# Performance work log

Hardware: AMD Instinct MI355X
Metric: run time of the kernel (lower is better)

The kernel has to match this reference:

```python
import jax, jax.numpy as jnp
import numpy as np

EPS = 1.1  # GIN epsilon from GINLayer(1.1, dim)
N_GIN = 4

def setup_inputs() -> dict:
    key = jax.random.key(0)
    ks = jax.random.split(key, 24)
    R, F_IN, H1, D = 1048576, 64, 256, 128
    N, E, B, A1, T = 100000, 1600000, 4096, 256, 16
    s = 0.05
    inp = {}
    inp['bulk'] = jax.random.normal(ks[0], (R, F_IN), dtype=jnp.float32)
    inp['seg_ids'] = jnp.sort(jax.random.randint(ks[1], (R,), 0, N))
    inp['edge_src'] = jax.random.randint(ks[2], (E,), 0, N)
    inp['edge_dst'] = jax.random.randint(ks[3], (E,), 0, N)
    inp['root_idx'] = jax.random.randint(ks[4], (B,), 0, N)
    inp['num_nodes'] = N
    # feature extractor: Linear(64,256)+ReLU, Linear(256,128)+ReLU
    inp['W1'] = jax.random.normal(ks[5], (F_IN, H1), dtype=jnp.float32) * s
    inp['b1'] = jnp.zeros((H1,), jnp.float32)
    inp['W2'] = jax.random.normal(ks[6], (H1, D), dtype=jnp.float32) * s
    inp['b2'] = jnp.zeros((D,), jnp.float32)
    # 4 GIN layers, dim D -> D
    inp['gin_W'] = jax.random.normal(ks[7], (N_GIN, D, D), dtype=jnp.float32) * s
    inp['gin_b'] = jnp.zeros((N_GIN, D), jnp.float32)
    # actor: Linear(128,256)+ReLU, Linear(256,16)+ReLU, Softmax
    inp['Wa1'] = jax.random.normal(ks[8], (D, A1), dtype=jnp.float32) * s
    inp['ba1'] = jnp.zeros((A1,), jnp.float32)
    inp['Wa2'] = jax.random.normal(ks[9], (A1, T), dtype=jnp.float32) * s
    inp['ba2'] = jnp.zeros((T,), jnp.float32)
    # critic: Linear(128,256)+ReLU, Linear(256,1)
    inp['Wc1'] = jax.random.normal(ks[10], (D, A1), dtype=jnp.float32) * s
    inp['bc1'] = jnp.zeros((A1,), jnp.float32)
    inp['Wc2'] = jax.random.normal(ks[11], (A1, 1), dtype=jnp.float32) * s
    inp['bc2'] = jnp.zeros((1,), jnp.float32)
    return inp

def reference(bulk, seg_ids, edge_src, edge_dst, root_idx, num_nodes,
              W1, b1, W2, b2, gin_W, gin_b, Wa1, ba1, Wa2, ba2, Wc1, bc1, Wc2, bc2):
    # feature extractor over all rows
    h = jax.nn.relu(bulk @ W1 + b1)
    h = jax.nn.relu(h @ W2 + b2)  # [R, D]
    # per-dataset mean aggregation (self.aggregator over split groups)
    sums = jax.ops.segment_sum(h, seg_ids, num_segments=num_nodes)
    counts = jax.ops.segment_sum(jnp.ones((h.shape[0],), h.dtype), seg_ids, num_segments=num_nodes)
    node_h = sums / jnp.maximum(counts, 1.0)[:, None]  # [N, D]
    # GIN message passing: h_v <- relu(W ((1+eps) h_v + sum_{child u} h_u) + b)
    for i in range(N_GIN):
        agg = jax.ops.segment_sum(node_h[edge_src], edge_dst, num_segments=num_nodes)
        node_h = jax.nn.relu(((1.0 + EPS) * node_h + agg) @ gin_W[i] + gin_b[i])
    X = node_h[root_idx]  # [B, D] current-node representations
    act = jax.nn.softmax(jax.nn.relu(jax.nn.relu(X @ Wa1 + ba1) @ Wa2 + ba2), axis=-1)
    crit = (jax.nn.relu(X @ Wc1 + bc1) @ Wc2 + bc2).squeeze(-1)
    return (act, crit)
```

## Files before the change

### kernel.cpp

```cpp
#include <hip/hip_runtime.h>
#include <math.h>

#define R_ROWS 1048576
#define F_IN   64
#define H1     256
#define D      128
#define NN     100000
#define NE     1600000
#define NB     4096
#define A1     256
#define NTOK   16
#define N_GIN  4
#define FE_ROWS 64

typedef short short8 __attribute__((ext_vector_type(8)));
typedef float f32x4  __attribute__((ext_vector_type(4)));
typedef unsigned int uintx4 __attribute__((ext_vector_type(4)));

__device__ __forceinline__ ushort f2bf(float x) {
    uint u = __builtin_bit_cast(uint, x);
    u += 0x7FFFu + ((u >> 16) & 1u);
    return (ushort)(u >> 16);
}
__device__ __forceinline__ float bf2f(ushort h) {
    uint u = ((uint)h) << 16;
    return __builtin_bit_cast(float, u);
}
__device__ __forceinline__ uint cvtpk(float lo, float hi) {
    uint r;
    asm("v_cvt_pk_bf16_f32 %0, %1, %2" : "=v"(r) : "v"(lo), "v"(hi));
    return r;
}
__device__ __forceinline__ float lo16f(uint p) { return __builtin_bit_cast(float, p << 16); }
__device__ __forceinline__ float hi16f(uint p) { return __builtin_bit_cast(float, p & 0xFFFF0000u); }

__device__ __forceinline__ f32x4 mm(short8 a, short8 b, f32x4 c) {
    return __builtin_amdgcn_mfma_f32_16x16x32_bf16(a, b, c, 0, 0, 0);
}
__device__ __forceinline__ void acc_add(f32x4& L, f32x4& H, const uintx4 p) {
    L[0] += lo16f(p[0]); H[0] += hi16f(p[0]);
    L[1] += lo16f(p[1]); H[1] += hi16f(p[1]);
    L[2] += lo16f(p[2]); H[2] += hi16f(p[2]);
    L[3] += lo16f(p[3]); H[3] += hi16f(p[3]);
}

__device__ __forceinline__ void pack_one(const float* __restrict__ W, int Ndim,
                                         int f, int lane, ushort* __restrict__ out)
{
    const int NTn = Ndim >> 4;
    const int kt = f / NTn, nt = f - kt * NTn;
    const int k0 = kt * 32 + (lane >> 4) * 8;
    const int n = nt * 16 + (lane & 15);
    uintx4 Hv, Lv;
    #pragma unroll
    for (int jj = 0; jj < 4; ++jj) {
        const float x0 = W[(k0 + 2 * jj) * Ndim + n];
        const float x1 = W[(k0 + 2 * jj + 1) * Ndim + n];
        const ushort h0 = f2bf(x0), l0 = f2bf(x0 - bf2f(h0));
        const ushort h1u = f2bf(x1), l1 = f2bf(x1 - bf2f(h1u));
        Hv[jj] = (uint)h0 | ((uint)h1u << 16);
        Lv[jj] = (uint)l0 | ((uint)l1 << 16);
    }
    *reinterpret_cast<uintx4*>(&out[((f * 2 + 0) * 64 + lane) * 8]) = Hv;
    *reinterpret_cast<uintx4*>(&out[((f * 2 + 1) * 64 + lane) * 8]) = Lv;
}

__global__ __launch_bounds__(256) void pack_all(
    const float* __restrict__ W1, const float* __restrict__ W2,
    const float* __restrict__ ginW, const float* __restrict__ Wa1,
    const float* __restrict__ Wc1, const float* __restrict__ Wa2,
    ushort* __restrict__ W1p, ushort* __restrict__ W2p, ushort* __restrict__ Gp,
    ushort* __restrict__ Wa1p, ushort* __restrict__ Wc1p, ushort* __restrict__ Wa2p,
    int* __restrict__ deg, int* __restrict__ mark, int* __restrict__ cnt)
{
    const int bid = blockIdx.x;
    if (bid < 90) {
        const int fid = bid * 4 + (threadIdx.x >> 6);
        const int lane = threadIdx.x & 63;
        if (fid < 32) pack_one(W1, H1, fid, lane, W1p);
        else if (fid < 96) pack_one(W2, D, fid - 32, lane, W2p);
        else if (fid < 224) {
            const int l = (fid - 96) >> 5;
            pack_one(ginW + (long)l * D * D, D, (fid - 96) & 31, lane, Gp + (long)l * 32768);
        } else if (fid < 288) pack_one(Wa1, A1, fid - 224, lane, Wa1p);
        else if (fid < 352) pack_one(Wc1, A1, fid - 288, lane, Wc1p);
        else if (fid < 360) pack_one(Wa2, NTOK, fid - 352, lane, Wa2p);
    } else {
        const int zb = bid - 90;
        const int idx0 = (zb * 256 + threadIdx.x) * 4;
        #pragma unroll
        for (int k = 0; k < 4; ++k) {
            const int idx = idx0 + k;
            if (idx < NN) deg[idx] = 0;
            else if (idx < 2 * NN) mark[idx - NN] = 0;
        }
        if (bid == 90 && threadIdx.x == 0) cnt[0] = 0;
    }
}

__global__ __launch_bounds__(256, 4) void fe_mfma(
    const float* __restrict__ bulk, const int* __restrict__ seg,
    const ushort* __restrict__ W1p, const float* __restrict__ b1,
    const ushort* __restrict__ W2p, const float* __restrict__ b2,
    float* __restrict__ sums)
{
    __shared__ __align__(16) uint smem_u[10240];
    char* Ab  = (char*)smem_u;
    char* h1b = Ab + 8192;
    float* h2 = (float*)smem_u;

    const int t = threadIdx.x;
    const int lane = t & 63;
    const int w = t >> 6;
    const long r0 = (long)blockIdx.x * FE_ROWS;

    #pragma unroll
    for (int i = 0; i < 4; ++i) {
        const int gid = t + i * 256;
        const int row = gid >> 4;
        const int c4 = (gid & 15) * 4;
        const float4 v = *reinterpret_cast<const float4*>(&bulk[(r0 + row) * F_IN + c4]);
        uint2 pk; pk.x = cvtpk(v.x, v.y); pk.y = cvtpk(v.z, v.w);
        const int byteoff = row * 128 + ((c4 * 2) ^ ((row & 7) << 4));
        *reinterpret_cast<uint2*>(Ab + byteoff) = pk;
    }
    __syncthreads();

    const f32x4 zz = {0.f, 0.f, 0.f, 0.f};
    f32x4 acc1[4][4];
    #pragma unroll
    for (int mtl = 0; mtl < 4; ++mtl)
        #pragma unroll
        for (int ntb = 0; ntb < 4; ++ntb) acc1[mtl][ntb] = zz;

    #pragma unroll
    for (int kt = 0; kt < 2; ++kt) {
        short8 aw[4];
        #pragma unroll
        for (int mtl = 0; mtl < 4; ++mtl) {
            const int f = kt * 16 + (w * 4 + mtl);
            aw[mtl] = *reinterpret_cast<const short8*>(&W1p[((f * 2 + 0) * 64 + lane) * 8]);
        }
        short8 bh[4];
        #pragma unroll
        for (int ntb = 0; ntb < 4; ++ntb) {
            const int row = ntb * 16 + (lane & 15);
            const int k0 = kt * 32 + (lane >> 4) * 8;
            bh[ntb] = *reinterpret_cast<const short8*>(Ab + (row * 128 + ((k0 * 2) ^ ((row & 7) << 4))));
        }
        #pragma unroll
        for (int mtl = 0; mtl < 4; ++mtl)
            #pragma unroll
            for (int ntb = 0; ntb < 4; ++ntb)
                acc1[mtl][ntb] = mm(aw[mtl], bh[ntb], acc1[mtl][ntb]);
    }

    #pragma unroll
    for (int mtl = 0; mtl < 4; ++mtl) {
        const int hcb = w * 64 + mtl * 16 + (lane >> 4) * 4;
        const float4 bv = *reinterpret_cast<const float4*>(&b1[hcb]);
        #pragma unroll
        for (int ntb = 0; ntb < 4; ++ntb) {
            const int hr = (lane & 15) + ntb * 16;
            const float v0 = fmaxf(acc1[mtl][ntb][0] + bv.x, 0.f);
            const float v1 = fmaxf(acc1[mtl][ntb][1] + bv.y, 0.f);
            const float v2 = fmaxf(acc1[mtl][ntb][2] + bv.z, 0.f);
            const float v3 = fmaxf(acc1[mtl][ntb][3] + bv.w, 0.f);
            uint2 pk; pk.x = cvtpk(v0, v1); pk.y = cvtpk(v2, v3);
            const int byteoff = (hr * 512 + hcb * 2) ^ ((hr & 7) << 4);
            *reinterpret_cast<uint2*>(h1b + byteoff) = pk;
        }
    }
    __syncthreads();

    float b2v[2];
    #pragma unroll
    for (int ntl = 0; ntl < 2; ++ntl) b2v[ntl] = b2[w * 32 + ntl * 16 + (lane & 15)];
    f32x4 acc2[4][2];
    #pragma unroll
    for (int mt = 0; mt < 4; ++mt) { acc2[mt][0] = zz; acc2[mt][1] = zz; }

    #pragma unroll
    for (int kt = 0; kt < 8; ++kt) {
        short8 bw2[2][2];
        #pragma unroll
        for (int ntl = 0; ntl < 2; ++ntl)
            #pragma unroll
            for (int p = 0; p < 2; ++p) {
                const int f = kt * 8 + (w * 2 + ntl);
                bw2[ntl][p] = *reinterpret_cast<const short8*>(&W2p[((f * 2 + p) * 64 + lane) * 8]);
            }
        short8 ah[4];
        #pragma unroll
        for (int mt = 0; mt < 4; ++mt) {
            const int row = mt * 16 + (lane & 15);
            const int k0 = kt * 32 + (lane >> 4) * 8;
            ah[mt] = *reinterpret_cast<const short8*>(h1b + ((row * 512 + k0 * 2) ^ ((row & 7) << 4)));
        }
        #pragma unroll
        for (int mt = 0; mt < 4; ++mt)
            #pragma unroll
            for (int ntl = 0; ntl < 2; ++ntl) {
                acc2[mt][ntl] = mm(ah[mt], bw2[ntl][0], acc2[mt][ntl]);
                acc2[mt][ntl] = mm(ah[mt], bw2[ntl][1], acc2[mt][ntl]);
            }
    }
    __syncthreads();

    #pragma unroll
    for (int mt = 0; mt < 4; ++mt)
        #pragma unroll
        for (int ntl = 0; ntl < 2; ++ntl)
            #pragma unroll
            for (int r = 0; r < 4; ++r) {
                const int row = mt * 16 + (lane >> 4) * 4 + r;
                const int col = w * 32 + ntl * 16 + (lane & 15);
                h2[row * 132 + col] = fmaxf(acc2[mt][ntl][r] + b2v[ntl], 0.f);
            }
    __syncthreads();

    {
        const int g = t >> 7;
        const int c = t & 127;
        const int base = g * 32;
        const long rb = r0 + base;
        const int prev = (rb == 0) ? -1 : seg[rb - 1];
        const int nxt = (rb + 32 >= R_ROWS) ? -1 : seg[rb + 32];
        int cur = seg[rb];
        float run = 0.f;
        int runstart = 0;
        #pragma unroll 1
        for (int r = 0; r < 32; ++r) {
            const int s = seg[rb + r];
            if (s != cur) {
                if (runstart != 0 || cur != prev) sums[(long)cur * D + c] = run;
                else atomicAdd(&sums[(long)cur * D + c], run);
                cur = s; run = 0.f; runstart = r;
            }
            run += h2[(base + r) * 132 + c];
        }
        if ((runstart != 0 || cur != prev) && cur != nxt) sums[(long)cur * D + c] = run;
        else atomicAdd(&sums[(long)cur * D + c], run);
    }
}

__global__ __launch_bounds__(256) void start_kernel(const int* __restrict__ seg,
                                                    int* __restrict__ start)
{
    const int n = blockIdx.x * 256 + threadIdx.x;
    if (n > NN) return;
    int lo = 0, hi = R_ROWS;
    #pragma unroll 1
    while (lo < hi) {
        const int mid = (lo + hi) >> 1;
        if (seg[mid] < n) lo = mid + 1; else hi = mid;
    }
    start[n] = lo;
}

__global__ __launch_bounds__(256) void divide_bf(
    const float* __restrict__ sums, const int* __restrict__ start,
    uint* __restrict__ hbf)
{
    const long i = (long)blockIdx.x * 256 + threadIdx.x;
    if (i < (long)NN * 64) {
        const int n = (int)(i >> 6), u = (int)(i & 63);
        const int cA = (u & 15) + (u >> 4) * 32;
        const float inv = 1.f / fmaxf((float)(start[n + 1] - start[n]), 1.f);
        const float vA = sums[(long)n * D + cA] * inv;
        const float vB = sums[(long)n * D + cA + 16] * inv;
        hbf[i] = cvtpk(vA, vB);
    }
}

__global__ __launch_bounds__(256) void hist_kernel(const int* __restrict__ edst,
                                                   int* __restrict__ deg)
{
    const int e = blockIdx.x * 256 + threadIdx.x;
    if (e < NE) atomicAdd(&deg[edst[e]], 1);
}

#define SCHUNK 2048
__global__ __launch_bounds__(256) void scan_reduce(const int* __restrict__ deg,
                                                   int* __restrict__ partials, int n)
{
    __shared__ int sdata[256];
    const int b = blockIdx.x, t = threadIdx.x;
    const int base = b * SCHUNK;
    int sum = 0;
    for (int i = t; i < SCHUNK; i += 256) {
        const int idx = base + i;
        sum += (idx < n) ? deg[idx] : 0;
    }
    sdata[t] = sum; __syncthreads();
    for (int s = 128; s > 0; s >>= 1) {
        if (t < s) sdata[t] += sdata[t + s];
        __syncthreads();
    }
    if (t == 0) partials[b] = sdata[0];
}

__global__ __launch_bounds__(256) void scan_write(const int* __restrict__ deg,
                                                  const int* __restrict__ partials,
                                                  int nchunks,
                                                  int* __restrict__ offsets,
                                                  int* __restrict__ cursor, int n)
{
    __shared__ int sdata[256];
    __shared__ int base_sh;
    const int b = blockIdx.x, t = threadIdx.x;
    if (t < 64) {
        int v = (t < b && t < nchunks) ? partials[t] : 0;
        #pragma unroll
        for (int d2 = 1; d2 < 64; d2 <<= 1) v += __shfl_xor(v, d2);
        if (t == 0) base_sh = v;
    }
    const int base = b * SCHUNK;
    int loc[8]; int s = 0;
    #pragma unroll
    for (int j = 0; j < 8; ++j) {
        const int idx = base + t * 8 + j;
        const int v = (idx < n) ? deg[idx] : 0;
        loc[j] = s; s += v;
    }
    sdata[t] = s; __syncthreads();
    for (int d = 1; d < 256; d <<= 1) {
        const int v = (t >= d) ? sdata[t - d] : 0;
        __syncthreads();
        sdata[t] += v;
        __syncthreads();
    }
    const int excl = (t == 0) ? 0 : sdata[t - 1];
    const int tbase = base_sh + excl;
    #pragma unroll
    for (int j = 0; j < 8; ++j) {
        const int idx = base + t * 8 + j;
        if (idx < n) {
            const int o = tbase + loc[j];
            offsets[idx] = o;
            cursor[idx] = o;
        }
    }
}

__global__ __launch_bounds__(256) void scatter_edges(const int* __restrict__ esrc,
                                                     const int* __restrict__ edst,
                                                     int* __restrict__ cursor,
                                                     int* __restrict__ csr_src)
{
    const int e = blockIdx.x * 256 + threadIdx.x;
    if (e < NE) {
        const int d = edst[e];
        const int p = atomicAdd(&cursor[d], 1);
        csr_src[p] = esrc[e];
    }
}

__global__ __launch_bounds__(256) void mark_kernel(
    const int* __restrict__ root, const int* __restrict__ offsets,
    const int* __restrict__ deg, const int* __restrict__ csr,
    int* __restrict__ mark)
{
    const int b = blockIdx.x * 256 + threadIdx.x;
    if (b < NB) {
        const int n = root[b];
        mark[n] = 1;
        const int off = offsets[n], dg = deg[n];
        for (int j = 0; j < dg; ++j) mark[csr[off + j]] = 1;
    }
}

__global__ __launch_bounds__(256) void compact_kernel(
    const int* __restrict__ mark, int* __restrict__ list, int* __restrict__ cnt)
{
    const int n = blockIdx.x * 256 + threadIdx.x;
    if (n < NN && mark[n]) {
        const int p = atomicAdd(cnt, 1);
        list[p] = n;
    }
}

template<int MODE>
__global__ __launch_bounds__(256, 8) void gin_kernel(
    const uint* __restrict__ hbf, const int* __restrict__ offsets,
    const int* __restrict__ deg, const int* __restrict__ csr,
    const ushort* __restrict__ Wp, const float* __restrict__ bvec,
    uint* __restrict__ outbuf,
    const int* __restrict__ list, const int* __restrict__ cnt,
    const int* __restrict__ root)
{
    __shared__ __align__(16) char ylds[64 * 256];
    __shared__ int nid[64];
    const int t = threadIdx.x, lane = t & 63, w = t >> 6;
    const int h = lane >> 5;
    const int q2 = (lane >> 4) & 1;
    const int m = lane & 15;
    const int q = lane >> 4;
    const int r0 = blockIdx.x * 64;
    const int CNT = (MODE == 1) ? cnt[0] : 0;
    if (MODE == 1 && r0 >= CNT) return;

    #pragma unroll 1
    for (int i = 0; i < 8; ++i) {
        const int row = w * 16 + i * 2 + h;
        int n = -1;
        if (MODE == 0) {
            const int nn = r0 + row;
            if (nn < NN) n = nn;
        } else if (MODE == 1) {
            const int idx = r0 + row;
            if (idx < CNT) n = list[idx];
        } else {
            n = root[r0 + row];
        }
        if (MODE == 1 && (lane & 31) == 0) nid[row] = n;
        f32x4 accL = {0.f, 0.f, 0.f, 0.f};
        f32x4 accH = {0.f, 0.f, 0.f, 0.f};
        if (n >= 0) {
            const uintx4 sp = *reinterpret_cast<const uintx4*>(&hbf[(long)n * 64 + 4 * m]);
            const float sc = (q2 == 0) ? 2.1f : 0.f;
            accL[0] = sc * lo16f(sp[0]); accH[0] = sc * hi16f(sp[0]);
            accL[1] = sc * lo16f(sp[1]); accH[1] = sc * hi16f(sp[1]);
            accL[2] = sc * lo16f(sp[2]); accH[2] = sc * hi16f(sp[2]);
            accL[3] = sc * lo16f(sp[3]); accH[3] = sc * hi16f(sp[3]);
            const int off = offsets[n];
            const int dg = deg[n];
            const int dg2 = dg >> 1;
            int jj = 0;
            for (; jj + 4 <= dg2; jj += 4) {
                const int b0 = off + 2 * jj + q2;
                const int s0 = csr[b0], s1 = csr[b0 + 2], s2 = csr[b0 + 4], s3 = csr[b0 + 6];
                const uintx4 p0 = *reinterpret_cast<const uintx4*>(&hbf[(long)s0 * 64 + 4 * m]);
                const uintx4 p1 = *reinterpret_cast<const uintx4*>(&hbf[(long)s1 * 64 + 4 * m]);
                const uintx4 p2 = *reinterpret_cast<const uintx4*>(&hbf[(long)s2 * 64 + 4 * m]);
                const uintx4 p3 = *reinterpret_cast<const uintx4*>(&hbf[(long)s3 * 64 + 4 * m]);
                acc_add(accL, accH, p0);
                acc_add(accL, accH, p1);
                acc_add(accL, accH, p2);
                acc_add(accL, accH, p3);
            }
            for (; jj < dg2; ++jj) {
                const int s = csr[off + 2 * jj + q2];
                const uintx4 p = *reinterpret_cast<const uintx4*>(&hbf[(long)s * 64 + 4 * m]);
                acc_add(accL, accH, p);
            }
            if ((dg & 1) && q2 == 0) {
                const int s = csr[off + dg - 1];
                const uintx4 p = *reinterpret_cast<const uintx4*>(&hbf[(long)s * 64 + 4 * m]);
                acc_add(accL, accH, p);
            }
        }
        #pragma unroll
        for (int e = 0; e < 4; ++e) {
            accL[e] += __shfl_xor(accL[e], 16);
            accH[e] += __shfl_xor(accH[e], 16);
        }
        const int swz = (row & 7) << 4;
        #pragma unroll
        for (int e = 0; e < 2; ++e) {
            const int u = 4 * m + 2 * q2 + e;
            const int cA = (u & 15) + (u >> 4) * 32;
            const uint pk = cvtpk(accL[2 * q2 + e], accH[2 * q2 + e]);
            *reinterpret_cast<ushort*>(ylds + ((row * 256 + cA * 2) ^ swz)) = (ushort)pk;
            *reinterpret_cast<ushort*>(ylds + ((row * 256 + (cA + 16) * 2) ^ swz)) = (ushort)(pk >> 16);
        }
    }

    short8 bw0[2];
    #pragma unroll
    for (int ntl = 0; ntl < 2; ++ntl) {
        const int f = w * 2 + ntl;
        bw0[ntl] = *reinterpret_cast<const short8*>(&Wp[((f * 2 + 0) * 64 + lane) * 8]);
    }
    __syncthreads();

    const f32x4 zz = {0.f, 0.f, 0.f, 0.f};
    f32x4 acc[4][2];
    #pragma unroll
    for (int mt = 0; mt < 4; ++mt) { acc[mt][0] = zz; acc[mt][1] = zz; }

    #pragma unroll
    for (int kt = 0; kt < 4; ++kt) {
        short8 bw[2];
        if (kt == 0) { bw[0] = bw0[0]; bw[1] = bw0[1]; }
        else {
            #pragma unroll
            for (int ntl = 0; ntl < 2; ++ntl) {
                const int f = kt * 8 + (w * 2 + ntl);
                bw[ntl] = *reinterpret_cast<const short8*>(&Wp[((f * 2 + 0) * 64 + lane) * 8]);
            }
        }
        #pragma unroll
        for (int mt = 0; mt < 4; ++mt) {
            const int row = mt * 16 + m;
            const int k0 = kt * 32 + q * 8;
            const short8 ah = *reinterpret_cast<const short8*>(
                ylds + ((row * 256 + k0 * 2) ^ ((row & 7) << 4)));
            acc[mt][0] = mm(ah, bw[0], acc[mt][0]);
            acc[mt][1] = mm(ah, bw[1], acc[mt][1]);
        }
    }

    const float bv0 = bvec[w * 32 + m];
    const float bv1 = bvec[w * 32 + 16 + m];
    #pragma unroll
    for (int mt = 0; mt < 4; ++mt)
        #pragma unroll
        for (int r = 0; r < 4; ++r) {
            const int grow_row = mt * 16 + q * 4 + r;
            const float v0 = fmaxf(acc[mt][0][r] + bv0, 0.f);
            const float v1 = fmaxf(acc[mt][1][r] + bv1, 0.f);
            const uint pk = cvtpk(v0, v1);
            if (MODE == 0) {
                const long nout = r0 + grow_row;
                if (nout < NN) outbuf[nout * 64 + w * 16 + m] = pk;
            } else if (MODE == 1) {
                if (r0 + grow_row < CNT) {
                    const long nout = nid[grow_row];
                    outbuf[nout * 64 + w * 16 + m] = pk;
                }
            } else {
                outbuf[(long)(r0 + grow_row) * 64 + w * 16 + m] = pk;
            }
        }
}

__global__ __launch_bounds__(256) void head_mfma(
    const uint* __restrict__ Xbf,
    const ushort* __restrict__ Wa1p, const float* __restrict__ ba1,
    const ushort* __restrict__ Wa2p, const float* __restrict__ ba2,
    const ushort* __restrict__ Wc1p, const float* __restrict__ bc1,
    const float* __restrict__ Wc2, const float* __restrict__ bc2,
    float* __restrict__ out_act, float* __restrict__ out_crit)
{
    __shared__ __align__(16) char Xp[64 * 256];
    __shared__ __align__(16) char a1p[64 * 512];
    const int t = threadIdx.x, lane = t & 63, w = t >> 6;
    const int r0 = blockIdx.x * 64;
    const f32x4 zz = {0.f, 0.f, 0.f, 0.f};

    {
        const int row = t >> 2;
        const int ug = (t & 3) * 16;
        const int swz = (row & 7) << 4;
        #pragma unroll
        for (int uu = 0; uu < 16; ++uu) {
            const uint pk = Xbf[(long)(r0 + row) * 64 + ug + uu];
            const int u = ug + uu;
            const int cA = (u & 15) + (u >> 4) * 32;
            *reinterpret_cast<ushort*>(Xp + ((row * 256 + cA * 2) ^ swz)) = (ushort)pk;
            *reinterpret_cast<ushort*>(Xp + ((row * 256 + (cA + 16) * 2) ^ swz)) = (ushort)(pk >> 16);
        }
    }
    __syncthreads();

    {
        f32x4 acc1[4][4];
        #pragma unroll
        for (int mtl = 0; mtl < 4; ++mtl)
            #pragma unroll
            for (int ntb = 0; ntb < 4; ++ntb) acc1[mtl][ntb] = zz;
        #pragma unroll
        for (int kt = 0; kt < 4; ++kt) {
            short8 aw[4][2];
            #pragma unroll
            for (int mtl = 0; mtl < 4; ++mtl)
                #pragma unroll
                for (int p = 0; p < 2; ++p) {
                    const int f = kt * 16 + (w * 4 + mtl);
                    aw[mtl][p] = *reinterpret_cast<const short8*>(&Wa1p[((f * 2 + p) * 64 + lane) * 8]);
                }
            short8 bh[4];
            #pragma unroll
            for (int ntb = 0; ntb < 4; ++ntb) {
                const int row = ntb * 16 + (lane & 15);
                const int k0 = kt * 32 + (lane >> 4) * 8;
                bh[ntb] = *reinterpret_cast<const short8*>(Xp + ((row * 256 + k0 * 2) ^ ((row & 7) << 4)));
            }
            #pragma unroll
            for (int mtl = 0; mtl < 4; ++mtl)
                #pragma unroll
                for (int ntb = 0; ntb < 4; ++ntb) {
                    acc1[mtl][ntb] = mm(aw[mtl][0], bh[ntb], acc1[mtl][ntb]);
                    acc1[mtl][ntb] = mm(aw[mtl][1], bh[ntb], acc1[mtl][ntb]);
                }
        }
        #pragma unroll
        for (int mtl = 0; mtl < 4; ++mtl) {
            const int hcb = w * 64 + mtl * 16 + (lane >> 4) * 4;
            const float4 bv = *reinterpret_cast<const float4*>(&ba1[hcb]);
            #pragma unroll
            for (int ntb = 0; ntb < 4; ++ntb) {
                const int hr = (lane & 15) + ntb * 16;
                const float v0 = fmaxf(acc1[mtl][ntb][0] + bv.x, 0.f);
                const float v1 = fmaxf(acc1[mtl][ntb][1] + bv.y, 0.f);
                const float v2 = fmaxf(acc1[mtl][ntb][2] + bv.z, 0.f);
                const float v3 = fmaxf(acc1[mtl][ntb][3] + bv.w, 0.f);
                uint2 pk; pk.x = cvtpk(v0, v1); pk.y = cvtpk(v2, v3);
                const int byteoff = (hr * 512 + hcb * 2) ^ ((hr & 7) << 4);
                *reinterpret_cast<uint2*>(a1p + byteoff) = pk;
            }
        }
    }
    __syncthreads();

    {
        f32x4 accl = zz;
        #pragma unroll
        for (int kt = 0; kt < 8; ++kt) {
            short8 b2h = *reinterpret_cast<const short8*>(&Wa2p[((kt * 2 + 0) * 64 + lane) * 8]);
            short8 b2l = *reinterpret_cast<const short8*>(&Wa2p[((kt * 2 + 1) * 64 + lane) * 8]);
            const int row = w * 16 + (lane & 15);
            const int k0 = kt * 32 + (lane >> 4) * 8;
            const short8 ah = *reinterpret_cast<const short8*>(a1p + ((row * 512 + k0 * 2) ^ ((row & 7) << 4)));
            accl = mm(ah, b2h, accl);
            accl = mm(ah, b2l, accl);
        }
        const int j = lane & 15;
        float lg[4], mx[4], sm[4];
        #pragma unroll
        for (int r = 0; r < 4; ++r) {
            lg[r] = fmaxf(accl[r] + ba2[j], 0.f);
            float m2 = lg[r];
            #pragma unroll
            for (int d2 = 1; d2 < 16; d2 <<= 1) m2 = fmaxf(m2, __shfl_xor(m2, d2));
            mx[r] = m2;
            lg[r] = expf(lg[r] - m2);
            float s2 = lg[r];
            #pragma unroll
            for (int d2 = 1; d2 < 16; d2 <<= 1) s2 += __shfl_xor(s2, d2);
            sm[r] = s2;
        }
        #pragma unroll
        for (int r = 0; r < 4; ++r) {
            const int root_slot = r0 + w * 16 + (lane >> 4) * 4 + r;
            out_act[(long)root_slot * NTOK + j] = lg[r] / sm[r];
        }
    }
    __syncthreads();

    {
        f32x4 acc1[4][4];
        #pragma unroll
        for (int mtl = 0; mtl < 4; ++mtl)
            #pragma unroll
            for (int ntb = 0; ntb < 4; ++ntb) acc1[mtl][ntb] = zz;
        #pragma unroll
        for (int kt = 0; kt < 4; ++kt) {
            short8 aw[4][2];
            #pragma unroll
            for (int mtl = 0; mtl < 4; ++mtl)
                #pragma unroll
                for (int p = 0; p < 2; ++p) {
                    const int f = kt * 16 + (w * 4 + mtl);
                    aw[mtl][p] = *reinterpret_cast<const short8*>(&Wc1p[((f * 2 + p) * 64 + lane) * 8]);
                }
            short8 bh[4];
            #pragma unroll
            for (int ntb = 0; ntb < 4; ++ntb) {
                const int row = ntb * 16 + (lane & 15);
                const int k0 = kt * 32 + (lane >> 4) * 8;
                bh[ntb] = *reinterpret_cast<const short8*>(Xp + ((row * 256 + k0 * 2) ^ ((row & 7) << 4)));
            }
            #pragma unroll
            for (int mtl = 0; mtl < 4; ++mtl)
                #pragma unroll
                for (int ntb = 0; ntb < 4; ++ntb) {
                    acc1[mtl][ntb] = mm(aw[mtl][0], bh[ntb], acc1[mtl][ntb]);
                    acc1[mtl][ntb] = mm(aw[mtl][1], bh[ntb], acc1[mtl][ntb]);
                }
        }
        #pragma unroll
        for (int mtl = 0; mtl < 4; ++mtl) {
            const int hcb = w * 64 + mtl * 16 + (lane >> 4) * 4;
            const float4 bv = *reinterpret_cast<const float4*>(&bc1[hcb]);
            #pragma unroll
            for (int ntb = 0; ntb < 4; ++ntb) {
                const int hr = (lane & 15) + ntb * 16;
                const float v0 = fmaxf(acc1[mtl][ntb][0] + bv.x, 0.f);
                const float v1 = fmaxf(acc1[mtl][ntb][1] + bv.y, 0.f);
                const float v2 = fmaxf(acc1[mtl][ntb][2] + bv.z, 0.f);
                const float v3 = fmaxf(acc1[mtl][ntb][3] + bv.w, 0.f);
                uint2 pk; pk.x = cvtpk(v0, v1); pk.y = cvtpk(v2, v3);
                const int byteoff = (hr * 512 + hcb * 2) ^ ((hr & 7) << 4);
                *reinterpret_cast<uint2*>(a1p + byteoff) = pk;
            }
        }
    }
    __syncthreads();

    {
        const int row = w * 16 + (lane & 15);
        const int qk = lane >> 4;
        float dot = 0.f;
        #pragma unroll
        for (int g = 0; g < 8; ++g) {
            const int k0 = qk * 64 + g * 8;
            const short8 av = *reinterpret_cast<const short8*>(a1p + ((row * 512 + k0 * 2) ^ ((row & 7) << 4)));
            #pragma unroll
            for (int e = 0; e < 8; ++e)
                dot = fmaf(bf2f((ushort)av[e]), Wc2[k0 + e], dot);
        }
        dot += __shfl_xor(dot, 16);
        dot += __shfl_xor(dot, 32);
        if (lane < 16) out_crit[r0 + w * 16 + lane] = dot + bc2[0];
    }
}

extern "C" void kernel_launch(void* const* d_in, const int* in_sizes, int n_in,
                              void* d_out, int out_size, void* d_ws, size_t ws_size,
                              hipStream_t stream)
{
    const float* bulk = (const float*)d_in[0];
    const int*   seg  = (const int*)d_in[1];
    const int*   esrc = (const int*)d_in[2];
    const int*   edst = (const int*)d_in[3];
    const int*   root = (const int*)d_in[4];
    const float* W1   = (const float*)d_in[6];
    const float* b1   = (const float*)d_in[7];
    const float* W2   = (const float*)d_in[8];
    const float* b2   = (const float*)d_in[9];
    const float* ginW = (const float*)d_in[10];
    const float* ginb = (const float*)d_in[11];
    const float* Wa1  = (const float*)d_in[12];
    const float* ba1  = (const float*)d_in[13];
    const float* Wa2  = (const float*)d_in[14];
    const float* ba2  = (const float*)d_in[15];
    const float* Wc1  = (const float*)d_in[16];
    const float* bc1  = (const float*)d_in[17];
    const float* Wc2  = (const float*)d_in[18];
    const float* bc2  = (const float*)d_in[19];

    char* ws = (char*)d_ws;
    ushort* W1p = (ushort*)ws;
    ushort* W2p = W1p + 32768;
    float* sums    = (float*)(ws + 196608);
    uint*  hbfA    = (uint*)(sums + (long)NN * D);
    uint*  hbfB    = hbfA + (long)NN * 64;
    int*   start   = (int*)(hbfB + (long)NN * 64);
    int*   deg     = start + (NN + 4);
    int*   offsets = deg + NN;
    int*   cursor  = offsets + NN;
    int*   partials= cursor + NN;
    int*   csr     = partials + 256;
    int*   mark    = csr + NE;
    int*   list    = mark + NN;
    int*   cnt     = list + NN;
    uint*  Xbf     = (uint*)(cnt + 4);
    ushort* Gp     = (ushort*)(Xbf + (long)NB * 64);
    ushort* Wa1p   = Gp + 4 * 32768;
    ushort* Wc1p   = Wa1p + 65536;
    ushort* Wa2p   = Wc1p + 65536;

    hipMemsetAsync(sums, 0, (long)NN * D * sizeof(float), stream);

    pack_all<<<286, 256, 0, stream>>>(W1, W2, ginW, Wa1, Wc1, Wa2,
                                      W1p, W2p, Gp, Wa1p, Wc1p, Wa2p,
                                      deg, mark, cnt);

    fe_mfma<<<R_ROWS / FE_ROWS, 256, 0, stream>>>(bulk, seg, W1p, b1, W2p, b2, sums);
    start_kernel<<<(NN + 256) / 256, 256, 0, stream>>>(seg, start);
    divide_bf<<<((long)NN * 64 + 255) / 256, 256, 0, stream>>>(sums, start, hbfA);

    hist_kernel<<<(NE + 255) / 256, 256, 0, stream>>>(edst, deg);
    const int nchunks = (NN + SCHUNK - 1) / SCHUNK;
    scan_reduce<<<nchunks, 256, 0, stream>>>(deg, partials, NN);
    scan_write<<<nchunks, 256, 0, stream>>>(deg, partials, nchunks, offsets, cursor, NN);
    scatter_edges<<<(NE + 255) / 256, 256, 0, stream>>>(esrc, edst, cursor, csr);

    mark_kernel<<<(NB + 255) / 256, 256, 0, stream>>>(root, offsets, deg, csr, mark);
    compact_kernel<<<(NN + 255) / 256, 256, 0, stream>>>(mark, list, cnt);

    const int full_grid = (NN + 63) / 64;
    gin_kernel<0><<<full_grid, 256, 0, stream>>>(hbfA, offsets, deg, csr,
        Gp + 0L * 32768, ginb + 0L * D, hbfB, list, cnt, root);
    gin_kernel<0><<<full_grid, 256, 0, stream>>>(hbfB, offsets, deg, csr,
        Gp + 1L * 32768, ginb + 1L * D, hbfA, list, cnt, root);
    gin_kernel<1><<<full_grid, 256, 0, stream>>>(hbfA, offsets, deg, csr,
        Gp + 2L * 32768, ginb + 2L * D, hbfB, list, cnt, root);
    gin_kernel<2><<<NB / 64, 256, 0, stream>>>(hbfB, offsets, deg, csr,
        Gp + 3L * 32768, ginb + 3L * D, Xbf, list, cnt, root);

    head_mfma<<<NB / 64, 256, 0, stream>>>(Xbf, Wa1p, ba1, Wa2p, ba2,
                                           Wc1p, bc1, Wc2, bc2,
                                           (float*)d_out, (float*)d_out + (long)NB * NTOK);
}
```

Baseline: 733.0 us.

## Load bulk directly into MFMA operands, drop W2 lo term, remove layer-3 pruning

```diff
diff --git a/kernel.cpp b/kernel.cpp
--- a/kernel.cpp
+++ b/kernel.cpp
@@ -43,6 +43,14 @@
     L[2] += lo16f(p[2]); H[2] += hi16f(p[2]);
     L[3] += lo16f(p[3]); H[3] += hi16f(p[3]);
 }
+__device__ __forceinline__ short8 load_bf8(const float* __restrict__ p) {
+    const float4 v0 = *reinterpret_cast<const float4*>(p);
+    const float4 v1 = *reinterpret_cast<const float4*>(p + 4);
+    uintx4 pk;
+    pk[0] = cvtpk(v0.x, v0.y); pk[1] = cvtpk(v0.z, v0.w);
+    pk[2] = cvtpk(v1.x, v1.y); pk[3] = cvtpk(v1.z, v1.w);
+    return __builtin_bit_cast(short8, pk);
+}
 
 __device__ __forceinline__ void pack_one(const float* __restrict__ W, int Ndim,
                                          int f, int lane, ushort* __restrict__ out)
@@ -71,7 +79,7 @@
     const float* __restrict__ Wc1, const float* __restrict__ Wa2,
     ushort* __restrict__ W1p, ushort* __restrict__ W2p, ushort* __restrict__ Gp,
     ushort* __restrict__ Wa1p, ushort* __restrict__ Wc1p, ushort* __restrict__ Wa2p,
-    int* __restrict__ deg, int* __restrict__ mark, int* __restrict__ cnt)
+    int* __restrict__ deg)
 {
     const int bid = blockIdx.x;
     if (bid < 90) {
@@ -92,9 +100,7 @@
         for (int k = 0; k < 4; ++k) {
             const int idx = idx0 + k;
             if (idx < NN) deg[idx] = 0;
-            else if (idx < 2 * NN) mark[idx - NN] = 0;
-        }
-        if (bid == 90 && threadIdx.x == 0) cnt[0] = 0;
+        }
     }
 }
 
@@ -104,28 +110,15 @@
     const ushort* __restrict__ W2p, const float* __restrict__ b2,
     float* __restrict__ sums)
 {
-    __shared__ __align__(16) uint smem_u[10240];
-    char* Ab  = (char*)smem_u;
-    char* h1b = Ab + 8192;
-    float* h2 = (float*)smem_u;
+    __shared__ __align__(16) uint smem_u[8448];
+    char*  h1b = (char*)smem_u;
+    float* h2  = (float*)smem_u;
 
     const int t = threadIdx.x;
     const int lane = t & 63;
     const int w = t >> 6;
     const long r0 = (long)blockIdx.x * FE_ROWS;
 
-    #pragma unroll
-    for (int i = 0; i < 4; ++i) {
-        const int gid = t + i * 256;
-        const int row = gid >> 4;
-        const int c4 = (gid & 15) * 4;
-        const float4 v = *reinterpret_cast<const float4*>(&bulk[(r0 + row) * F_IN + c4]);
-        uint2 pk; pk.x = cvtpk(v.x, v.y); pk.y = cvtpk(v.z, v.w);
-        const int byteoff = row * 128 + ((c4 * 2) ^ ((row & 7) << 4));
-        *reinterpret_cast<uint2*>(Ab + byteoff) = pk;
-    }
-    __syncthreads();
-
     const f32x4 zz = {0.f, 0.f, 0.f, 0.f};
     f32x4 acc1[4][4];
     #pragma unroll
@@ -146,7 +139,7 @@
         for (int ntb = 0; ntb < 4; ++ntb) {
             const int row = ntb * 16 + (lane & 15);
             const int k0 = kt * 32 + (lane >> 4) * 8;
-            bh[ntb] = *reinterpret_cast<const short8*>(Ab + (row * 128 + ((k0 * 2) ^ ((row & 7) << 4))));
+            bh[ntb] = load_bf8(&bulk[(r0 + row) * F_IN + k0]);
         }
         #pragma unroll
         for (int mtl = 0; mtl < 4; ++mtl)
@@ -182,14 +175,12 @@
 
     #pragma unroll
     for (int kt = 0; kt < 8; ++kt) {
-        short8 bw2[2][2];
-        #pragma unroll
-        for (int ntl = 0; ntl < 2; ++ntl)
-            #pragma unroll
-            for (int p = 0; p < 2; ++p) {
-                const int f = kt * 8 + (w * 2 + ntl);
-                bw2[ntl][p] = *reinterpret_cast<const short8*>(&W2p[((f * 2 + p) * 64 + lane) * 8]);
-            }
+        short8 bw2[2];
+        #pragma unroll
+        for (int ntl = 0; ntl < 2; ++ntl) {
+            const int f = kt * 8 + (w * 2 + ntl);
+            bw2[ntl] = *reinterpret_cast<const short8*>(&W2p[((f * 2 + 0) * 64 + lane) * 8]);
+        }
         short8 ah[4];
         #pragma unroll
         for (int mt = 0; mt < 4; ++mt) {
@@ -200,10 +191,8 @@
         #pragma unroll
         for (int mt = 0; mt < 4; ++mt)
             #pragma unroll
-            for (int ntl = 0; ntl < 2; ++ntl) {
-                acc2[mt][ntl] = mm(ah[mt], bw2[ntl][0], acc2[mt][ntl]);
-                acc2[mt][ntl] = mm(ah[mt], bw2[ntl][1], acc2[mt][ntl]);
-            }
+            for (int ntl = 0; ntl < 2; ++ntl)
+                acc2[mt][ntl] = mm(ah[mt], bw2[ntl], acc2[mt][ntl]);
     }
     __syncthreads();
 
@@ -356,49 +345,20 @@
     }
 }
 
-__global__ __launch_bounds__(256) void mark_kernel(
-    const int* __restrict__ root, const int* __restrict__ offsets,
-    const int* __restrict__ deg, const int* __restrict__ csr,
-    int* __restrict__ mark)
-{
-    const int b = blockIdx.x * 256 + threadIdx.x;
-    if (b < NB) {
-        const int n = root[b];
-        mark[n] = 1;
-        const int off = offsets[n], dg = deg[n];
-        for (int j = 0; j < dg; ++j) mark[csr[off + j]] = 1;
-    }
-}
-
-__global__ __launch_bounds__(256) void compact_kernel(
-    const int* __restrict__ mark, int* __restrict__ list, int* __restrict__ cnt)
-{
-    const int n = blockIdx.x * 256 + threadIdx.x;
-    if (n < NN && mark[n]) {
-        const int p = atomicAdd(cnt, 1);
-        list[p] = n;
-    }
-}
-
 template<int MODE>
 __global__ __launch_bounds__(256, 8) void gin_kernel(
     const uint* __restrict__ hbf, const int* __restrict__ offsets,
     const int* __restrict__ deg, const int* __restrict__ csr,
     const ushort* __restrict__ Wp, const float* __restrict__ bvec,
-    uint* __restrict__ outbuf,
-    const int* __restrict__ list, const int* __restrict__ cnt,
-    const int* __restrict__ root)
+    uint* __restrict__ outbuf, const int* __restrict__ root)
 {
     __shared__ __align__(16) char ylds[64 * 256];
-    __shared__ int nid[64];
     const int t = threadIdx.x, lane = t & 63, w = t >> 6;
     const int h = lane >> 5;
     const int q2 = (lane >> 4) & 1;
     const int m = lane & 15;
     const int q = lane >> 4;
     const int r0 = blockIdx.x * 64;
-    const int CNT = (MODE == 1) ? cnt[0] : 0;
-    if (MODE == 1 && r0 >= CNT) return;
 
     #pragma unroll 1
     for (int i = 0; i < 8; ++i) {
@@ -407,13 +367,9 @@
         if (MODE == 0) {
             const int nn = r0 + row;
             if (nn < NN) n = nn;
-        } else if (MODE == 1) {
-            const int idx = r0 + row;
-            if (idx < CNT) n = list[idx];
         } else {
             n = root[r0 + row];
         }
-        if (MODE == 1 && (lane & 31) == 0) nid[row] = n;
         f32x4 accL = {0.f, 0.f, 0.f, 0.f};
         f32x4 accH = {0.f, 0.f, 0.f, 0.f};
         if (n >= 0) {
@@ -514,11 +470,6 @@
             if (MODE == 0) {
                 const long nout = r0 + grow_row;
                 if (nout < NN) outbuf[nout * 64 + w * 16 + m] = pk;
-            } else if (MODE == 1) {
-                if (r0 + grow_row < CNT) {
-                    const long nout = nid[grow_row];
-                    outbuf[nout * 64 + w * 16 + m] = pk;
-                }
             } else {
                 outbuf[(long)(r0 + grow_row) * 64 + w * 16 + m] = pk;
             }
@@ -617,14 +568,13 @@
             accl = mm(ah, b2l, accl);
         }
         const int j = lane & 15;
-        float lg[4], mx[4], sm[4];
+        float lg[4], sm[4];
         #pragma unroll
         for (int r = 0; r < 4; ++r) {
             lg[r] = fmaxf(accl[r] + ba2[j], 0.f);
             float m2 = lg[r];
             #pragma unroll
             for (int d2 = 1; d2 < 16; d2 <<= 1) m2 = fmaxf(m2, __shfl_xor(m2, d2));
-            mx[r] = m2;
             lg[r] = expf(lg[r] - m2);
             float s2 = lg[r];
             #pragma unroll
@@ -743,10 +693,7 @@
     int*   cursor  = offsets + NN;
     int*   partials= cursor + NN;
     int*   csr     = partials + 256;
-    int*   mark    = csr + NE;
-    int*   list    = mark + NN;
-    int*   cnt     = list + NN;
-    uint*  Xbf     = (uint*)(cnt + 4);
+    uint*  Xbf     = (uint*)(csr + NE);
     ushort* Gp     = (ushort*)(Xbf + (long)NB * 64);
     ushort* Wa1p   = Gp + 4 * 32768;
     ushort* Wc1p   = Wa1p + 65536;
@@ -754,9 +701,8 @@
 
     hipMemsetAsync(sums, 0, (long)NN * D * sizeof(float), stream);
 
-    pack_all<<<286, 256, 0, stream>>>(W1, W2, ginW, Wa1, Wc1, Wa2,
-                                      W1p, W2p, Gp, Wa1p, Wc1p, Wa2p,
-                                      deg, mark, cnt);
+    pack_all<<<188, 256, 0, stream>>>(W1, W2, ginW, Wa1, Wc1, Wa2,
+                                      W1p, W2p, Gp, Wa1p, Wc1p, Wa2p, deg);
 
     fe_mfma<<<R_ROWS / FE_ROWS, 256, 0, stream>>>(bulk, seg, W1p, b1, W2p, b2, sums);
     start_kernel<<<(NN + 256) / 256, 256, 0, stream>>>(seg, start);
@@ -768,18 +714,15 @@
     scan_write<<<nchunks, 256, 0, stream>>>(deg, partials, nchunks, offsets, cursor, NN);
     scatter_edges<<<(NE + 255) / 256, 256, 0, stream>>>(esrc, edst, cursor, csr);
 
-    mark_kernel<<<(NB + 255) / 256, 256, 0, stream>>>(root, offsets, deg, csr, mark);
-    compact_kernel<<<(NN + 255) / 256, 256, 0, stream>>>(mark, list, cnt);
-
     const int full_grid = (NN + 63) / 64;
     gin_kernel<0><<<full_grid, 256, 0, stream>>>(hbfA, offsets, deg, csr,
-        Gp + 0L * 32768, ginb + 0L * D, hbfB, list, cnt, root);
+        Gp + 0L * 32768, ginb + 0L * D, hbfB, root);
     gin_kernel<0><<<full_grid, 256, 0, stream>>>(hbfB, offsets, deg, csr,
-        Gp + 1L * 32768, ginb + 1L * D, hbfA, list, cnt, root);
-    gin_kernel<1><<<full_grid, 256, 0, stream>>>(hbfA, offsets, deg, csr,
-        Gp + 2L * 32768, ginb + 2L * D, hbfB, list, cnt, root);
+        Gp + 1L * 32768, ginb + 1L * D, hbfA, root);
+    gin_kernel<0><<<full_grid, 256, 0, stream>>>(hbfA, offsets, deg, csr,
+        Gp + 2L * 32768, ginb + 2L * D, hbfB, root);
     gin_kernel<2><<<NB / 64, 256, 0, stream>>>(hbfB, offsets, deg, csr,
-        Gp + 3L * 32768, ginb + 3L * D, Xbf, list, cnt, root);
+        Gp + 3L * 32768, ginb + 3L * D, Xbf, root);
 
     head_mfma<<<NB / 64, 256, 0, stream>>>(Xbf, Wa1p, ba1, Wa2p, ba2,
                                            Wc1p, bc1, Wc2, bc2,
```

Result: slower. 789.5 us (+7.7%).
